# Kernel optimization log

Measured on AMD Instinct MI355X. Metric: run time of the kernel, lower is better.

## Reference

```python
import jax, jax.numpy as jnp
import numpy as np

B, T, D = 512, 200, 512

def setup_inputs() -> dict:
    key = jax.random.key(0)
    k1, k2, k3 = jax.random.split(key, 3)
    inputs = jax.random.normal(k1, (B, T, D), dtype=jnp.float32)
    # Keras 'uniform' initializer -> U(-0.05, 0.05)
    W = jax.random.uniform(k2, (T, T), minval=-0.05, maxval=0.05, dtype=jnp.float32)
    b = jax.random.uniform(k3, (T,), minval=-0.05, maxval=0.05, dtype=jnp.float32)
    return {"inputs": inputs, "W": W, "b": b}

def reference(inputs, W, b):
    # x = permute(inputs, (0,2,1)) -> [B, D, T]; scores over timestep axis
    # a = softmax(tanh(x @ W + b)) along last axis (T)
    scores = jnp.tanh(jnp.einsum('btd,ts->bds', inputs, W) + b)  # [B, D, T]
    a = jax.nn.softmax(scores, axis=-1)                           # softmax over T
    # permute back to [B, T, D], elementwise multiply, sum over T -> [B, D]
    out = jnp.einsum('bdt,btd->bd', a, inputs)
    return out
```

## Files before the change

### kernel.cpp

```cpp
#include <hip/hip_runtime.h>
#include <cstdint>
#include <cstddef>

#define B_DIM 512
#define T_DIM 200
#define D_DIM 512
#define NPAD  208
#define NKG   28
#define NT    13
#define DT    64
#define KS_STEPS 7

typedef short  short8  __attribute__((ext_vector_type(8)));
typedef float  floatx4 __attribute__((ext_vector_type(4)));

__device__ __forceinline__ unsigned short f2bf(float f) {
  unsigned int u = __float_as_uint(f);
  u += 0x7fffu + ((u >> 16) & 1u);
  return (unsigned short)(u >> 16);
}
__device__ __forceinline__ float bf2f(unsigned short h) {
  return __uint_as_float(((unsigned int)h) << 16);
}

__global__ void prep_w_kernel(const float* __restrict__ W,
                              unsigned short* __restrict__ wf) {
  int idx = blockIdx.x * blockDim.x + threadIdx.x;
  if (idx >= NKG * 8 * NPAD) return;
  int k = idx / NPAD;
  int n = idx - k * NPAD;
  float v = (k < T_DIM && n < T_DIM) ? W[k * T_DIM + n] : 0.0f;
  wf[((size_t)(k >> 3) * NPAD + n) * 8 + (k & 7)] = f2bf(v);
}

__global__ __launch_bounds__(256, 4)
void attn_kernel(const float* __restrict__ X,
                 const unsigned short* __restrict__ wf,
                 const float* __restrict__ bias,
                 float* __restrict__ out) {
  __shared__ unsigned short Xa[NKG * DT * 8];

  const int tid = threadIdx.x;
  const int bb  = blockIdx.x >> 3;
  const int d0  = (blockIdx.x & 7) * DT;

  {
    const int m = tid & (DT - 1);
    const int q = tid >> 6;
    for (int kk = q; kk < NKG; kk += 4) {
      unsigned short pk[8];
      if (kk < 25) {
        const float* g = X + ((size_t)bb * T_DIM + (size_t)kk * 8) * D_DIM + d0 + m;
        #pragma unroll
        for (int j = 0; j < 8; ++j) pk[j] = f2bf(g[(size_t)j * D_DIM]);
      } else {
        #pragma unroll
        for (int j = 0; j < 8; ++j) pk[j] = 0;
      }
      int4 w;
      w.x = (int)pk[0] | ((int)pk[1] << 16);
      w.y = (int)pk[2] | ((int)pk[3] << 16);
      w.z = (int)pk[4] | ((int)pk[5] << 16);
      w.w = (int)pk[6] | ((int)pk[7] << 16);
      *(int4*)(&Xa[(kk * DT + m) * 8]) = w;
    }
  }
  __syncthreads();

  const int lane = tid & 63;
  const int l15  = lane & 15;
  const int g    = lane >> 4;
  const int wv   = tid >> 6;

  float bv[NT];
  #pragma unroll
  for (int nt = 0; nt < NT; ++nt) {
    int n = nt * 16 + l15;
    bv[nt] = (n < T_DIM) ? bias[n] : 0.0f;
  }

  floatx4 acc[NT];
  #pragma unroll
  for (int nt = 0; nt < NT; ++nt)
    acc[nt] = (floatx4){0.f, 0.f, 0.f, 0.f};

  for (int ks = 0; ks < KS_STEPS; ++ks) {
    const int kg = ks * 4 + g;
    short8 a = *(const short8*)(&Xa[(kg * DT + wv * 16 + l15) * 8]);
    const unsigned short* wp = wf + ((size_t)kg * NPAD + l15) * 8;
    #pragma unroll
    for (int nt = 0; nt < NT; ++nt) {
      short8 bfr = *(const short8*)(wp + nt * 16 * 8);
      acc[nt] = __builtin_amdgcn_mfma_f32_16x16x32_bf16(a, bfr, acc[nt], 0, 0, 0);
    }
  }

  float part[4] = {0.f, 0.f, 0.f, 0.f};
  float rs[4]   = {0.f, 0.f, 0.f, 0.f};
  #pragma unroll
  for (int nt = 0; nt < NT; ++nt) {
    const int t = nt * 16 + l15;
    const bool valid = (t < T_DIM);
    const unsigned short* xp = &Xa[((t >> 3) * DT) * 8 + (t & 7)];
    #pragma unroll
    for (int r = 0; r < 4; ++r) {
      if (valid) {
        float z  = acc[nt][r] + bv[nt];
        float e  = __expf(2.0f * z);
        float th = 1.0f - __fdividef(2.0f, e + 1.0f);
        float p  = __expf(th);
        rs[r]   += p;
        const int m = wv * 16 + g * 4 + r;
        part[r] += p * bf2f(xp[m * 8]);
      }
    }
  }
  #pragma unroll
  for (int off = 1; off <= 8; off <<= 1)
    #pragma unroll
    for (int r = 0; r < 4; ++r) {
      part[r] += __shfl_xor(part[r], off, 16);
      rs[r]   += __shfl_xor(rs[r],   off, 16);
    }

  if (l15 == 0) {
    #pragma unroll
    for (int r = 0; r < 4; ++r)
      out[(size_t)bb * D_DIM + d0 + wv * 16 + g * 4 + r] = part[r] * __frcp_rn(rs[r]);
  }
}

extern "C" void kernel_launch(void* const* d_in, const int* in_sizes, int n_in,
                              void* d_out, int out_size, void* d_ws, size_t ws_size,
                              hipStream_t stream) {
  const float* X  = (const float*)d_in[0];
  const float* W  = (const float*)d_in[1];
  const float* bs = (const float*)d_in[2];
  float* out = (float*)d_out;
  unsigned short* wf = (unsigned short*)d_ws;

  const int wtot = NKG * 8 * NPAD;
  hipLaunchKernelGGL(prep_w_kernel, dim3((wtot + 255) / 256), dim3(256), 0, stream,
                     W, wf);
  hipLaunchKernelGGL(attn_kernel, dim3(B_DIM * (D_DIM / DT)), dim3(256), 0, stream,
                     X, wf, bs, out);
}
```

Baseline: 347.5 us.

## Make each wave stage its own X tile with register prefetch, drop block sync

Each wave now handles an independent 16-column slice of d and loads its own X tile into a private LDS region. The global loads are software-pipelined through registers (loading the next k-group while converting and storing the current one), and the block-wide __syncthreads is removed. Occupancy hint raised to 5 and bias loads moved into the epilogue to save registers. The trade-off is narrower 64-byte global load segments per wave and possible register pressure from the prefetch buffers.

```diff
diff --git a/kernel.cpp b/kernel.cpp
--- a/kernel.cpp
+++ b/kernel.cpp
@@ -8,7 +8,6 @@
 #define NPAD  208
 #define NKG   28
 #define NT    13
-#define DT    64
 #define KS_STEPS 7
 
 typedef short  short8  __attribute__((ext_vector_type(8)));
@@ -33,50 +32,52 @@
   wf[((size_t)(k >> 3) * NPAD + n) * 8 + (k & 7)] = f2bf(v);
 }
 
-__global__ __launch_bounds__(256, 4)
+__global__ __launch_bounds__(256, 5)
 void attn_kernel(const float* __restrict__ X,
                  const unsigned short* __restrict__ wf,
                  const float* __restrict__ bias,
                  float* __restrict__ out) {
-  __shared__ unsigned short Xa[NKG * DT * 8];
+  __shared__ __align__(16) unsigned short Xa[4 * NKG * 16 * 8];
 
-  const int tid = threadIdx.x;
-  const int bb  = blockIdx.x >> 3;
-  const int d0  = (blockIdx.x & 7) * DT;
-
-  {
-    const int m = tid & (DT - 1);
-    const int q = tid >> 6;
-    for (int kk = q; kk < NKG; kk += 4) {
-      unsigned short pk[8];
-      if (kk < 25) {
-        const float* g = X + ((size_t)bb * T_DIM + (size_t)kk * 8) * D_DIM + d0 + m;
-        #pragma unroll
-        for (int j = 0; j < 8; ++j) pk[j] = f2bf(g[(size_t)j * D_DIM]);
-      } else {
-        #pragma unroll
-        for (int j = 0; j < 8; ++j) pk[j] = 0;
-      }
-      int4 w;
-      w.x = (int)pk[0] | ((int)pk[1] << 16);
-      w.y = (int)pk[2] | ((int)pk[3] << 16);
-      w.z = (int)pk[4] | ((int)pk[5] << 16);
-      w.w = (int)pk[6] | ((int)pk[7] << 16);
-      *(int4*)(&Xa[(kk * DT + m) * 8]) = w;
-    }
-  }
-  __syncthreads();
-
+  const int tid  = threadIdx.x;
+  const int wv   = tid >> 6;
   const int lane = tid & 63;
   const int l15  = lane & 15;
   const int g    = lane >> 4;
-  const int wv   = tid >> 6;
 
-  float bv[NT];
+  const int gw = blockIdx.x * 4 + wv;
+  const int bb = gw >> 5;
+  const int d0 = (gw & 31) << 4;
+
+  unsigned short* Xw = Xa + wv * (NKG * 16 * 8);
+  const float* xbase = X + (size_t)bb * T_DIM * D_DIM + d0 + l15;
+
+  float cur[8], nxt[8];
+  {
+    const float* p = xbase + (size_t)(g * 8) * D_DIM;
+    #pragma unroll
+    for (int j = 0; j < 8; ++j) cur[j] = p[(size_t)j * D_DIM];
+  }
   #pragma unroll
-  for (int nt = 0; nt < NT; ++nt) {
-    int n = nt * 16 + l15;
-    bv[nt] = (n < T_DIM) ? bias[n] : 0.0f;
+  for (int ks = 0; ks < KS_STEPS; ++ks) {
+    if (ks < 6) {
+      if (ks < 5 || g == 0) {
+        const float* p = xbase + (size_t)((ks + 1) * 32 + g * 8) * D_DIM;
+        #pragma unroll
+        for (int j = 0; j < 8; ++j) nxt[j] = p[(size_t)j * D_DIM];
+      } else {
+        #pragma unroll
+        for (int j = 0; j < 8; ++j) nxt[j] = 0.0f;
+      }
+    }
+    int4 w;
+    w.x = (int)f2bf(cur[0]) | ((int)f2bf(cur[1]) << 16);
+    w.y = (int)f2bf(cur[2]) | ((int)f2bf(cur[3]) << 16);
+    w.z = (int)f2bf(cur[4]) | ((int)f2bf(cur[5]) << 16);
+    w.w = (int)f2bf(cur[6]) | ((int)f2bf(cur[7]) << 16);
+    *(int4*)&Xw[(((ks * 4 + g) * 16) + l15) * 8] = w;
+    #pragma unroll
+    for (int j = 0; j < 8; ++j) cur[j] = nxt[j];
   }
 
   floatx4 acc[NT];
@@ -84,9 +85,10 @@
   for (int nt = 0; nt < NT; ++nt)
     acc[nt] = (floatx4){0.f, 0.f, 0.f, 0.f};
 
+  #pragma unroll
   for (int ks = 0; ks < KS_STEPS; ++ks) {
     const int kg = ks * 4 + g;
-    short8 a = *(const short8*)(&Xa[(kg * DT + wv * 16 + l15) * 8]);
+    short8 a = *(const short8*)&Xw[((kg * 16) + l15) * 8];
     const unsigned short* wp = wf + ((size_t)kg * NPAD + l15) * 8;
     #pragma unroll
     for (int nt = 0; nt < NT; ++nt) {
@@ -101,16 +103,17 @@
   for (int nt = 0; nt < NT; ++nt) {
     const int t = nt * 16 + l15;
     const bool valid = (t < T_DIM);
-    const unsigned short* xp = &Xa[((t >> 3) * DT) * 8 + (t & 7)];
+    const float bvn = valid ? bias[t] : 0.0f;
+    const unsigned short* xp = &Xw[((t >> 3) * 16) * 8 + (t & 7)];
     #pragma unroll
     for (int r = 0; r < 4; ++r) {
       if (valid) {
-        float z  = acc[nt][r] + bv[nt];
+        float z  = acc[nt][r] + bvn;
         float e  = __expf(2.0f * z);
         float th = 1.0f - __fdividef(2.0f, e + 1.0f);
         float p  = __expf(th);
         rs[r]   += p;
-        const int m = wv * 16 + g * 4 + r;
+        const int m = g * 4 + r;
         part[r] += p * bf2f(xp[m * 8]);
       }
     }
@@ -126,7 +129,7 @@
   if (l15 == 0) {
     #pragma unroll
     for (int r = 0; r < 4; ++r)
-      out[(size_t)bb * D_DIM + d0 + wv * 16 + g * 4 + r] = part[r] * __frcp_rn(rs[r]);
+      out[(size_t)bb * D_DIM + d0 + g * 4 + r] = part[r] * __frcp_rn(rs[r]);
   }
 }
 
@@ -142,6 +145,6 @@
   const int wtot = NKG * 8 * NPAD;
   hipLaunchKernelGGL(prep_w_kernel, dim3((wtot + 255) / 256), dim3(256), 0, stream,
                      W, wf);
-  hipLaunchKernelGGL(attn_kernel, dim3(B_DIM * (D_DIM / DT)), dim3(256), 0, stream,
+  hipLaunchKernelGGL(attn_kernel, dim3(4096), dim3(256), 0, stream,
                      X, wf, bs, out);
 }
```

New measurement: 405.4 us. +16.7%, slower.
